# Kernel optimization log

Measured on AMD Instinct MI355X. Metric: run time of the kernel, lower is better.

## Reference

```python
import jax, jax.numpy as jnp
import numpy as np
from jax import lax

B = 8192
HS = 64        # hidden_size (output channels)
HS4 = HS + 4   # internal channel count (68)
K = 3          # conv kernel size


def setup_inputs() -> dict:
    key = jax.random.key(0)
    ks = jax.random.split(key, 16)
    def n(k, shape, s=1.0):
        return jax.random.normal(k, shape, dtype=jnp.float32) * s
    return {
        "x": n(ks[0], (B, HS, 6, 6)),
        "cell": n(ks[1], (B, 2)),
        "interspace_coord": n(ks[2], (B, 2, 6, 6)),
        "conv1_w": n(ks[3], (HS4, HS4, K, K), 0.05),
        "conv1_b": n(ks[4], (HS4,), 0.05),
        "conv3_w": n(ks[5], (HS4, HS4, K, K), 0.05),
        "conv3_b": n(ks[6], (HS4,), 0.05),
        "lin5_w": n(ks[7], (9 * HS, HS4 * 25), 0.02),
        "lin5_b": n(ks[8], (9 * HS,), 0.02),
        "lin4_w": n(ks[9], (9 * HS, HS4 * 16), 0.02),
        "lin4_b": n(ks[10], (9 * HS,), 0.02),
        "lin3_w": n(ks[11], (9 * HS, HS4 * 9), 0.02),
        "lin3_b": n(ks[12], (9 * HS,), 0.02),
        "final_w": n(ks[13], (HS, 9 * HS), 0.02),
        "final_b": n(ks[14], (HS,), 0.02),
    }


def _conv(z, w, b):
    # torch Conv2d with padding=k//2, stride 1 == SAME conv, NCHW/OIHW
    y = lax.conv_general_dilated(z, w, (1, 1), 'SAME',
                                 dimension_numbers=('NCHW', 'OIHW', 'NCHW'))
    return y + b[None, :, None, None]


def _corners(z, ws):
    # four corner windows, stacked on a new leading axis (corner-major)
    H, W = z.shape[-2:]
    return jnp.stack([z[..., :ws, :ws],
                      z[..., :ws, W - ws:],
                      z[..., H - ws:, :ws],
                      z[..., H - ws:, W - ws:]], axis=0)


def reference(x, cell, interspace_coord,
              conv1_w, conv1_b, conv3_w, conv3_b,
              lin5_w, lin5_b, lin4_w, lin4_b, lin3_w, lin3_b,
              final_w, final_b):
    Bn = x.shape[0]
    new_cell = jnp.broadcast_to(cell.reshape(Bn, -1)[:, :, None, None],
                                (Bn, 2, 6, 6))
    lins = {5: (lin5_w, lin5_b), 4: (lin4_w, lin4_b), 3: (lin3_w, lin3_b)}
    for ws in (5, 4, 3):
        z = jnp.concatenate([x, new_cell, interspace_coord], axis=1)  # [B,68,6,6]
        z = _corners(z, ws).reshape(-1, HS4, ws, ws)                  # [4B,68,ws,ws]
        z = jnp.sin(z) + jnp.cos(z)
        z = jax.nn.relu(_conv(z, conv1_w, conv1_b))
        z = jnp.sin(z) + jnp.cos(z)
        z = jax.nn.relu(_conv(z, conv3_w, conv3_b)).reshape(4, Bn, -1)
        Wl, bl = lins[ws]
        z = jax.nn.relu(z @ Wl.T + bl).reshape(4, Bn, HS, 3, 3)
        m = jnp.concatenate([z[0], z[1]], axis=-1)   # [B,64,3,6]
        n = jnp.concatenate([z[2], z[3]], axis=-1)
        x = jnp.concatenate([m, n], axis=-2)          # [B,64,6,6]
    ew = 3
    c = _corners(x, ew)                               # [4,B,64,3,3]
    c = c.reshape(4 * Bn, -1) @ final_w.T + final_b   # [4B,64]
    c = c.reshape(Bn, HS, 2, 2)                       # same flat-order reshape as torch
    xc = x[:, :, ew - 1:ew + 1, ew - 1:ew + 1]        # center 2x2
    return (xc * c).reshape(Bn, HS, -1)
```

## Files before the change

kernel.cpp:

```cpp
#include <hip/hip_runtime.h>
#include <hip/hip_bf16.h>
#include <cstdint>
#include <cstddef>

#define BN 8192
#define MTOT 32768

using bf16 = __hip_bfloat16;
typedef float f32x4 __attribute__((ext_vector_type(4)));
typedef short short8 __attribute__((ext_vector_type(8)));

__device__ __forceinline__ bf16 f2b(float v) { return __float2bfloat16(v); }
__device__ __forceinline__ float b2f(bf16 v) { return __bfloat162float(v); }
__device__ __forceinline__ float sincos_sum(float x) {
    return 1.41421356237f * __sinf(x + 0.78539816340f);
}

template<int WS> struct WsCfg;
template<> struct WsCfg<5> { static constexpr int KD = 1728, NP = 1792, KTRUE = 1700; };
template<> struct WsCfg<4> { static constexpr int KD = 1088, NP = 1152, KTRUE = 1088; };
template<> struct WsCfg<3> { static constexpr int KD = 640,  NP = 640,  KTRUE = 612;  };

template<int WS, bool SRC_F32>
__global__ __launch_bounds__(256)
void zprep_block(const float* __restrict__ xF, const bf16* __restrict__ xB,
                 const float* __restrict__ cell, const float* __restrict__ isc,
                 bf16* __restrict__ Z, int m0g, int CM)
{
    constexpr int KD = WsCfg<WS>::KD;
    constexpr int KTRUE = 68 * WS * WS;
    const int b = blockIdx.x, tid = threadIdx.x;
    __shared__ float s[68][37];

    for (int i = tid; i < 64 * 36; i += 256) {
        int ic = i / 36, off = i % 36;
        size_t idx = ((size_t)b * 64 + ic) * 36 + off;
        float t = SRC_F32 ? xF[idx] : b2f(xB[idx]);
        s[ic][off] = sincos_sum(t);
    }
    if (tid < 2) {
        float t = sincos_sum(cell[b * 2 + tid]);
        #pragma unroll
        for (int off = 0; off < 36; off++) s[64 + tid][off] = t;
    }
    if (tid >= 64 && tid < 136) {
        int j = tid - 64;
        int ic = j / 36, off = j % 36;
        s[66 + ic][off] = sincos_sum(isc[((size_t)b * 2 + ic) * 36 + off]);
    }
    __syncthreads();

    for (int i = tid; i < 4 * KD; i += 256) {
        int q = i / KD, k = i % KD;
        int gm = q * BN + b;
        if (gm < m0g || gm >= m0g + CM) continue;
        float v = 0.f;
        if (k < KTRUE) {
            int pi = k / 68, ic = k % 68;
            int r = (q >> 1) * (6 - WS) + pi / WS;
            int c = (q & 1) * (6 - WS) + pi % WS;
            v = s[ic][r * 6 + c];
        }
        Z[(size_t)(gm - m0g) * KD + k] = f2b(v);
    }
}

template<int WS>
__global__ void build_wdense(const float* __restrict__ w1, const float* __restrict__ w3,
                             bf16* __restrict__ W1d, bf16* __restrict__ W3d)
{
    constexpr int KD = WsCfg<WS>::KD, NP = WsCfg<WS>::NP;
    constexpr int KTRUE = 68 * WS * WS;
    constexpr unsigned per = (unsigned)NP * (unsigned)KD;
    unsigned e = blockIdx.x * 256u + threadIdx.x;
    if (e >= 2u * per) return;
    const float* src = (e < per) ? w1 : w3;
    bf16* dst = (e < per) ? W1d : W3d;
    unsigned i = (e < per) ? e : (e - per);
    int n = (int)(i / (unsigned)KD), k = (int)(i % (unsigned)KD);
    float v = 0.f;
    if (n < KTRUE && k < KTRUE) {
        int po = n / 68, oc = n % 68, ro = po / WS, co = po % WS;
        int pi = k / 68, ic = k % 68, ri = pi / WS, ci = pi % WS;
        int kr = ri - ro + 1, kc = ci - co + 1;
        if (kr >= 0 && kr < 3 && kc >= 0 && kc < 3)
            v = src[((oc * 68 + ic) * 3 + kr) * 3 + kc];
    }
    dst[i] = f2b(v);
}

template<int WS>
__global__ void repack_lin(const float* __restrict__ wl, bf16* __restrict__ WlP)
{
    constexpr int KD = WsCfg<WS>::KD;
    constexpr int KTRUE = 68 * WS * WS;
    unsigned e = blockIdx.x * 256u + threadIdx.x;
    if (e >= 640u * (unsigned)KD) return;
    int n = (int)(e / (unsigned)KD), k = (int)(e % (unsigned)KD);
    float v = 0.f;
    if (n < 576 && k < KTRUE) {
        int pi = k / 68, ic = k % 68;
        v = wl[(size_t)n * KTRUE + ic * (WS * WS) + pi];
    }
    WlP[e] = f2b(v);
}

__global__ void repack_fin(const float* __restrict__ fw, bf16* __restrict__ WfP)
{
    unsigned e = blockIdx.x * 256u + threadIdx.x;
    if (e >= 128u * 576u) return;
    unsigned n = e / 576u, k = e % 576u;
    WfP[e] = (n < 64u) ? f2b(fw[n * 576u + k]) : f2b(0.f);
}

__global__ void build_bias(const float* __restrict__ b1, const float* __restrict__ b3,
                           const float* __restrict__ bl5, const float* __restrict__ bl4,
                           const float* __restrict__ bl3, const float* __restrict__ bfin,
                           float* __restrict__ bias)
{
    int e = blockIdx.x * 256 + threadIdx.x;
    if (e >= 9216) return;
    float v = 0.f;
    if (e < 1792)      { int n = e;        if (n < 1700) v = b1[n % 68]; }
    else if (e < 3584) { int n = e - 1792; if (n < 1700) v = b3[n % 68]; }
    else if (e < 4736) { int n = e - 3584; if (n < 1088) v = b1[n % 68]; }
    else if (e < 5888) { int n = e - 4736; if (n < 1088) v = b3[n % 68]; }
    else if (e < 6528) { int n = e - 5888; if (n < 612)  v = b1[n % 68]; }
    else if (e < 7168) { int n = e - 6528; if (n < 612)  v = b3[n % 68]; }
    else if (e < 7808) { int n = e - 7168; if (n < 576)  v = bl5[n]; }
    else if (e < 8448) { int n = e - 7808; if (n < 576)  v = bl4[n]; }
    else if (e < 9088) { int n = e - 8448; if (n < 576)  v = bl3[n]; }
    else               { int n = e - 9088; if (n < 64)   v = bfin[n]; }
    bias[e] = v;
}

__device__ __forceinline__ void gload_lds16(const bf16* g, const bf16* lds_wave_base)
{
    unsigned off = (unsigned)(uintptr_t)lds_wave_base;
    off = __builtin_amdgcn_readfirstlane(off);
    __builtin_amdgcn_global_load_lds((const __attribute__((address_space(1))) unsigned int*)g,
                                     (__attribute__((address_space(3))) unsigned int*)off,
                                     16, 0, 0);
}

__device__ __forceinline__ int imin(int a, int b) { return a < b ? a : b; }
__device__ __forceinline__ int imax(int a, int b) { return a > b ? a : b; }

template<int EPI, int WS>
__global__ __launch_bounds__(256)
void gemm_bt(const bf16* __restrict__ A, const bf16* __restrict__ Bm, int KD,
             const float* __restrict__ bias, int ntiles,
             bf16* __restrict__ C, int ldc, int nlimit,
             int m0g, bf16* __restrict__ xbuf_out,
             const bf16* __restrict__ afin_xc, float* __restrict__ outp)
{
    __shared__ bf16 As[128 * 32];
    __shared__ bf16 Bs[128 * 32];
    const int tid = threadIdx.x;
    const int wave = tid >> 6, lane = tid & 63;
    const int l15 = lane & 15, lq = lane >> 4;
    const int wr = (wave >> 1) * 64, wc = (wave & 1) * 64;

    const int id = blockIdx.x;
    const int mt8 = (int)gridDim.x / (ntiles * 8);
    const int xcd = id & 7, local = id >> 3;
    const int m_idx = xcd * mt8 + local / ntiles;
    const int n_idx = local % ntiles;
    const int n0 = n_idx * 128, m0 = m_idx * 128;

    int nspans = 1, sbeg[4], send[4];
    sbeg[0] = 0; send[0] = KD;
    if (WS > 0) {
        int po_lo = imin(n0 / 68, WS * WS - 1);
        int po_hi = imin((n0 + 127) / 68, WS * WS - 1);
        int ro_lo = po_lo / WS, ro_hi = po_hi / WS;
        int r_lo = imax(ro_lo - 1, 0), r_hi = imin(ro_hi + 1, WS - 1);
        int ci_lo = 0, ci_hi = WS - 1;
        if (ro_lo == ro_hi) {
            ci_lo = imax(po_lo % WS - 1, 0);
            ci_hi = imin(po_hi % WS + 1, WS - 1);
        }
        if (ci_lo == 0 && ci_hi == WS - 1) {
            sbeg[0] = (r_lo * WS * 68) & ~31;
            send[0] = imin(KD, ((r_hi + 1) * WS * 68 + 31) & ~31);
        } else {
            nspans = 0;
            for (int ri = r_lo; ri <= r_hi; ri++) {
                sbeg[nspans] = ((ri * WS + ci_lo) * 68) & ~31;
                send[nspans] = imin(KD, (((ri * WS + ci_hi + 1) * 68) + 31) & ~31);
                nspans++;
            }
        }
    }

    float bj[4];
    #pragma unroll
    for (int j = 0; j < 4; j++) bj[j] = bias[n0 + wc + j * 16 + l15];

    const bf16* Ab = A + (size_t)m0 * KD;
    const bf16* Bb = Bm + (size_t)n0 * KD;
    const int srow = tid >> 2, scol = (tid & 3) * 8;
    const bf16* aG0 = Ab + (size_t)srow * KD + scol;
    const bf16* aG1 = Ab + (size_t)(srow + 64) * KD + scol;
    const bf16* bG0 = Bb + (size_t)srow * KD + scol;
    const bf16* bG1 = Bb + (size_t)(srow + 64) * KD + scol;
    const bf16* lA0 = &As[wave * 512];
    const bf16* lA1 = &As[2048 + wave * 512];
    const bf16* lB0 = &Bs[wave * 512];
    const bf16* lB1 = &Bs[2048 + wave * 512];

    f32x4 acc[4][4];
    #pragma unroll
    for (int i = 0; i < 4; i++)
        #pragma unroll
        for (int j = 0; j < 4; j++) { f32x4 z = {0.f, 0.f, 0.f, 0.f}; acc[i][j] = z; }

    for (int s = 0; s < nspans; s++) {
        for (int k0 = sbeg[s]; k0 < send[s]; k0 += 32) {
            gload_lds16(aG0 + k0, lA0);
            gload_lds16(aG1 + k0, lA1);
            gload_lds16(bG0 + k0, lB0);
            gload_lds16(bG1 + k0, lB1);
            __syncthreads();
            short8 af[4], bg[4];
            #pragma unroll
            for (int i = 0; i < 4; i++) af[i] = *(const short8*)&As[(wr + i * 16 + l15) * 32 + lq * 8];
            #pragma unroll
            for (int j = 0; j < 4; j++) bg[j] = *(const short8*)&Bs[(wc + j * 16 + l15) * 32 + lq * 8];
            #pragma unroll
            for (int i = 0; i < 4; i++)
                #pragma unroll
                for (int j = 0; j < 4; j++)
                    acc[i][j] = __builtin_amdgcn_mfma_f32_16x16x32_bf16(af[i], bg[j], acc[i][j], 0, 0, 0);
            __syncthreads();
        }
    }

    #pragma unroll
    for (int i = 0; i < 4; i++) {
        #pragma unroll
        for (int j = 0; j < 4; j++) {
            int n = n0 + wc + j * 16 + l15;
            #pragma unroll
            for (int r = 0; r < 4; r++) {
                int m = m0 + wr + i * 16 + lq * 4 + r;
                float v = acc[i][j][r];
                if (EPI == 0) {
                    if (n < nlimit) {
                        v += bj[j]; v = fmaxf(v, 0.f); v = sincos_sum(v);
                        C[(size_t)m * ldc + n] = f2b(v);
                    }
                } else if (EPI == 1) {
                    if (n < nlimit) {
                        v += bj[j]; v = fmaxf(v, 0.f);
                        C[(size_t)m * ldc + n] = f2b(v);
                    }
                } else if (EPI == 2) {
                    if (n < 576) {
                        v += bj[j]; v = fmaxf(v, 0.f);
                        int gm = m0g + m;
                        int q = gm >> 13, b = gm & (BN - 1);
                        int ch = n / 9, p = n % 9, rr = p / 3, cc = p % 3;
                        int R = rr + (q >> 1) * 3, Cc = cc + (q & 1) * 3;
                        xbuf_out[((size_t)b * 64 + ch) * 36 + R * 6 + Cc] = f2b(v);
                    }
                } else {
                    if (n < 64) {
                        v += bj[j];
                        int gm = m0g + m;
                        int f = gm * 64 + n;
                        int b2 = f >> 8, rem = f & 255;
                        int ch2 = rem >> 2, ii = (rem >> 1) & 1, jj = rem & 1;
                        int qq = ii * 2 + jj;
                        const int offt[4] = {8, 6, 2, 0};
                        float xc = b2f(afin_xc[((size_t)qq * BN + b2) * 576 + ch2 * 9 + offt[qq]]);
                        outp[f] = v * xc;
                    }
                }
            }
        }
    }
}

template<int WS, bool SRC_F32>
static void run_ws(const float* xsrcF, const bf16* xsrcB, bf16* xdst, bf16* afin,
                   const float* cell, const float* isc,
                   bf16* Za, bf16* Zb, const bf16* W1d, const bf16* W3d, const bf16* WlP,
                   const float* bias, int bo1, int bo3, int bol,
                   int nchunk, hipStream_t stream)
{
    constexpr int KD = WsCfg<WS>::KD, NP = WsCfg<WS>::NP;
    int CM = MTOT / nchunk;
    int mt = CM / 128;
    for (int c = 0; c < nchunk; c++) {
        int m0g = c * CM;
        zprep_block<WS, SRC_F32><<<BN, 256, 0, stream>>>(
            xsrcF, xsrcB, cell, isc, Za, m0g, CM);
        int nt12 = NP / 128;
        gemm_bt<0, WS><<<nt12 * mt, 256, 0, stream>>>(Za, W1d, KD, bias + bo1, nt12,
                                                      Zb, KD, KD, 0, nullptr, nullptr, nullptr);
        gemm_bt<1, WS><<<nt12 * mt, 256, 0, stream>>>(Zb, W3d, KD, bias + bo3, nt12,
                                                      Za, KD, KD, 0, nullptr, nullptr, nullptr);
        if (afin) {
            gemm_bt<1, 0><<<5 * mt, 256, 0, stream>>>(Za, WlP, KD, bias + bol, 5,
                                                      afin + (size_t)m0g * 576, 576, 576,
                                                      0, nullptr, nullptr, nullptr);
        } else {
            gemm_bt<2, 0><<<5 * mt, 256, 0, stream>>>(Za, WlP, KD, bias + bol, 5,
                                                      nullptr, 0, 0, m0g, xdst, nullptr, nullptr);
        }
    }
}

extern "C" void kernel_launch(void* const* d_in, const int* in_sizes, int n_in,
                              void* d_out, int out_size, void* d_ws, size_t ws_size,
                              hipStream_t stream)
{
    const float* x    = (const float*)d_in[0];
    const float* cell = (const float*)d_in[1];
    const float* isc  = (const float*)d_in[2];
    const float* c1w  = (const float*)d_in[3];
    const float* c1b  = (const float*)d_in[4];
    const float* c3w  = (const float*)d_in[5];
    const float* c3b  = (const float*)d_in[6];
    const float* l5w  = (const float*)d_in[7];
    const float* l5b  = (const float*)d_in[8];
    const float* l4w  = (const float*)d_in[9];
    const float* l4b  = (const float*)d_in[10];
    const float* l3w  = (const float*)d_in[11];
    const float* l3b  = (const float*)d_in[12];
    const float* fw   = (const float*)d_in[13];
    const float* fb   = (const float*)d_in[14];

    char* base = (char*)d_ws;
    size_t cur = 0;
    auto take = [&](size_t bytes) -> char* {
        char* r = base + cur; cur += (bytes + 255) & ~(size_t)255; return r;
    };

    const size_t XB = (size_t)BN * 64 * 36 * 2;
    const size_t AFB = (size_t)MTOT * 576 * 2;
    size_t wbytes = 2 * (1792ull * 1728 + 1152ull * 1088 + 640ull * 640) * 2
                  + (640ull * 1728 + 640ull * 1088 + 640ull * 640) * 2
                  + 128ull * 576 * 2 + 9216ull * 4 + 64 * 256;
    auto need = [&](int nc) -> size_t {
        size_t xb = (nc > 1) ? 2 * XB : XB;
        return xb + AFB + wbytes + 2 * ((size_t)(MTOT / nc) * 1728 * 2);
    };
    int nchunk = (ws_size >= need(1)) ? 1 : (ws_size >= need(2)) ? 2
               : (ws_size >= need(4)) ? 4 : 8;

    bf16* xbufA = (bf16*)take(XB);
    bf16* xbufB = (nchunk > 1) ? (bf16*)take(XB) : xbufA;
    bf16* afinb = (bf16*)take(AFB);
    bf16* w1d5 = (bf16*)take(1792ull * 1728 * 2);
    bf16* w3d5 = (bf16*)take(1792ull * 1728 * 2);
    bf16* w1d4 = (bf16*)take(1152ull * 1088 * 2);
    bf16* w3d4 = (bf16*)take(1152ull * 1088 * 2);
    bf16* w1d3 = (bf16*)take(640ull * 640 * 2);
    bf16* w3d3 = (bf16*)take(640ull * 640 * 2);
    bf16* wl5p = (bf16*)take(640ull * 1728 * 2);
    bf16* wl4p = (bf16*)take(640ull * 1088 * 2);
    bf16* wl3p = (bf16*)take(640ull * 640 * 2);
    bf16* wfp  = (bf16*)take(128ull * 576 * 2);
    float* biasb = (float*)take(9216ull * 4);
    int CM = MTOT / nchunk;
    bf16* Za = (bf16*)take((size_t)CM * 1728 * 2);
    bf16* Zb = (bf16*)take((size_t)CM * 1728 * 2);

    auto nb = [](size_t t) { return dim3((unsigned)((t + 255) / 256)); };
    build_wdense<5><<<nb(2ull * 1792 * 1728), 256, 0, stream>>>(c1w, c3w, w1d5, w3d5);
    build_wdense<4><<<nb(2ull * 1152 * 1088), 256, 0, stream>>>(c1w, c3w, w1d4, w3d4);
    build_wdense<3><<<nb(2ull * 640 * 640), 256, 0, stream>>>(c1w, c3w, w1d3, w3d3);
    repack_lin<5><<<nb(640ull * 1728), 256, 0, stream>>>(l5w, wl5p);
    repack_lin<4><<<nb(640ull * 1088), 256, 0, stream>>>(l4w, wl4p);
    repack_lin<3><<<nb(640ull * 640), 256, 0, stream>>>(l3w, wl3p);
    repack_fin<<<nb(128ull * 576), 256, 0, stream>>>(fw, wfp);
    build_bias<<<36, 256, 0, stream>>>(c1b, c3b, l5b, l4b, l3b, fb, biasb);

    run_ws<5, true >(x, nullptr, xbufA, nullptr, cell, isc, Za, Zb, w1d5, w3d5, wl5p,
                     biasb, 0, 1792, 7168, nchunk, stream);
    run_ws<4, false>(nullptr, xbufA, xbufB, nullptr, cell, isc, Za, Zb, w1d4, w3d4, wl4p,
                     biasb, 3584, 4736, 7808, nchunk, stream);
    run_ws<3, false>(nullptr, xbufB, nullptr, afinb, cell, isc, Za, Zb, w1d3, w3d3, wl3p,
                     biasb, 5888, 6528, 8448, nchunk, stream);

    for (int c = 0; c < nchunk; c++) {
        int m0g = c * CM;
        int mt = CM / 128;
        gemm_bt<3, 0><<<mt, 256, 0, stream>>>(afinb + (size_t)m0g * 576, wfp, 576,
                                              biasb + 9088, 1, nullptr, 0, 0, m0g,
                                              nullptr, afinb, (float*)d_out);
    }
}
```

Before: 1.340 ms.

## Scatter linear epilogue directly into next stage's im2col buffer, merge setup kernels

```diff
diff --git a/kernel.cpp b/kernel.cpp
--- a/kernel.cpp
+++ b/kernel.cpp
@@ -21,22 +21,18 @@
 template<> struct WsCfg<4> { static constexpr int KD = 1088, NP = 1152, KTRUE = 1088; };
 template<> struct WsCfg<3> { static constexpr int KD = 640,  NP = 640,  KTRUE = 612;  };
 
-template<int WS, bool SRC_F32>
 __global__ __launch_bounds__(256)
-void zprep_block(const float* __restrict__ xF, const bf16* __restrict__ xB,
-                 const float* __restrict__ cell, const float* __restrict__ isc,
-                 bf16* __restrict__ Z, int m0g, int CM)
-{
-    constexpr int KD = WsCfg<WS>::KD;
-    constexpr int KTRUE = 68 * WS * WS;
+void zprep_block(const float* __restrict__ xF, const float* __restrict__ cell,
+                 const float* __restrict__ isc, bf16* __restrict__ Z,
+                 int m0g, int CM)
+{
+    constexpr int KD = 1728, KTRUE = 1700;
     const int b = blockIdx.x, tid = threadIdx.x;
     __shared__ float s[68][37];
 
     for (int i = tid; i < 64 * 36; i += 256) {
         int ic = i / 36, off = i % 36;
-        size_t idx = ((size_t)b * 64 + ic) * 36 + off;
-        float t = SRC_F32 ? xF[idx] : b2f(xB[idx]);
-        s[ic][off] = sincos_sum(t);
+        s[ic][off] = sincos_sum(xF[((size_t)b * 64 + ic) * 36 + off]);
     }
     if (tid < 2) {
         float t = sincos_sum(cell[b * 2 + tid]);
@@ -57,81 +53,136 @@
         float v = 0.f;
         if (k < KTRUE) {
             int pi = k / 68, ic = k % 68;
-            int r = (q >> 1) * (6 - WS) + pi / WS;
-            int c = (q & 1) * (6 - WS) + pi % WS;
+            int r = (q >> 1) + pi / 5;
+            int c = (q & 1) + pi % 5;
             v = s[ic][r * 6 + c];
         }
         Z[(size_t)(gm - m0g) * KD + k] = f2b(v);
     }
 }
 
-template<int WS>
-__global__ void build_wdense(const float* __restrict__ w1, const float* __restrict__ w3,
-                             bf16* __restrict__ W1d, bf16* __restrict__ W3d)
-{
-    constexpr int KD = WsCfg<WS>::KD, NP = WsCfg<WS>::NP;
-    constexpr int KTRUE = 68 * WS * WS;
-    constexpr unsigned per = (unsigned)NP * (unsigned)KD;
-    unsigned e = blockIdx.x * 256u + threadIdx.x;
-    if (e >= 2u * per) return;
-    const float* src = (e < per) ? w1 : w3;
-    bf16* dst = (e < per) ? W1d : W3d;
-    unsigned i = (e < per) ? e : (e - per);
-    int n = (int)(i / (unsigned)KD), k = (int)(i % (unsigned)KD);
+template<int WSv>
+__device__ __forceinline__ bf16 conv_elem(const float* __restrict__ src, int n, int k)
+{
+    constexpr int KTRUE = 68 * WSv * WSv;
     float v = 0.f;
     if (n < KTRUE && k < KTRUE) {
-        int po = n / 68, oc = n % 68, ro = po / WS, co = po % WS;
-        int pi = k / 68, ic = k % 68, ri = pi / WS, ci = pi % WS;
+        int po = n / 68, oc = n % 68, ro = po / WSv, co = po % WSv;
+        int pi = k / 68, ic = k % 68, ri = pi / WSv, ci = pi % WSv;
         int kr = ri - ro + 1, kc = ci - co + 1;
         if (kr >= 0 && kr < 3 && kc >= 0 && kc < 3)
             v = src[((oc * 68 + ic) * 3 + kr) * 3 + kc];
     }
-    dst[i] = f2b(v);
-}
-
-template<int WS>
-__global__ void repack_lin(const float* __restrict__ wl, bf16* __restrict__ WlP)
-{
-    constexpr int KD = WsCfg<WS>::KD;
-    constexpr int KTRUE = 68 * WS * WS;
-    unsigned e = blockIdx.x * 256u + threadIdx.x;
-    if (e >= 640u * (unsigned)KD) return;
-    int n = (int)(e / (unsigned)KD), k = (int)(e % (unsigned)KD);
+    return f2b(v);
+}
+template<int WSv>
+__device__ __forceinline__ bf16 lin_elem(const float* __restrict__ wl, int n, int k)
+{
+    constexpr int KTRUE = 68 * WSv * WSv;
     float v = 0.f;
     if (n < 576 && k < KTRUE) {
         int pi = k / 68, ic = k % 68;
-        v = wl[(size_t)n * KTRUE + ic * (WS * WS) + pi];
-    }
-    WlP[e] = f2b(v);
-}
-
-__global__ void repack_fin(const float* __restrict__ fw, bf16* __restrict__ WfP)
-{
+        v = wl[(size_t)n * KTRUE + ic * (WSv * WSv) + pi];
+    }
+    return f2b(v);
+}
+
+__global__ void megabuild(const float* __restrict__ c1w, const float* __restrict__ c3w,
+                          const float* __restrict__ l5w, const float* __restrict__ l4w,
+                          const float* __restrict__ l3w, const float* __restrict__ fw,
+                          const float* __restrict__ c1b, const float* __restrict__ c3b,
+                          const float* __restrict__ bl5, const float* __restrict__ bl4,
+                          const float* __restrict__ bl3, const float* __restrict__ bfin,
+                          const float* __restrict__ cell, const float* __restrict__ isc,
+                          bf16* __restrict__ w1d5, bf16* __restrict__ w3d5,
+                          bf16* __restrict__ w1d4, bf16* __restrict__ w3d4,
+                          bf16* __restrict__ w1d3, bf16* __restrict__ w3d3,
+                          bf16* __restrict__ wl5p, bf16* __restrict__ wl4p,
+                          bf16* __restrict__ wl3p, bf16* __restrict__ wfp,
+                          float* __restrict__ bias,
+                          bf16* __restrict__ Z4, bf16* __restrict__ Z3)
+{
+    constexpr unsigned S0 = 2u*1792*1728, S1 = 2u*1152*1088, S2 = 2u*640*640;
+    constexpr unsigned S3 = 640u*1728, S4 = 640u*1088, S5 = 640u*640;
+    constexpr unsigned S6 = 128u*576, S7 = 9216;
+    constexpr unsigned S8 = 4u*8192*16*4, S9 = 4u*8192*9*4, S10 = 32768u*28;
+    constexpr unsigned O1=S0, O2=O1+S1, O3=O2+S2, O4=O3+S3, O5=O4+S4, O6=O5+S5,
+                       O7=O6+S6, O8=O7+S7, O9=O8+S8, O10=O9+S9, OT=O10+S10;
     unsigned e = blockIdx.x * 256u + threadIdx.x;
-    if (e >= 128u * 576u) return;
-    unsigned n = e / 576u, k = e % 576u;
-    WfP[e] = (n < 64u) ? f2b(fw[n * 576u + k]) : f2b(0.f);
-}
-
-__global__ void build_bias(const float* __restrict__ b1, const float* __restrict__ b3,
-                           const float* __restrict__ bl5, const float* __restrict__ bl4,
-                           const float* __restrict__ bl3, const float* __restrict__ bfin,
-                           float* __restrict__ bias)
-{
-    int e = blockIdx.x * 256 + threadIdx.x;
-    if (e >= 9216) return;
-    float v = 0.f;
-    if (e < 1792)      { int n = e;        if (n < 1700) v = b1[n % 68]; }
-    else if (e < 3584) { int n = e - 1792; if (n < 1700) v = b3[n % 68]; }
-    else if (e < 4736) { int n = e - 3584; if (n < 1088) v = b1[n % 68]; }
-    else if (e < 5888) { int n = e - 4736; if (n < 1088) v = b3[n % 68]; }
-    else if (e < 6528) { int n = e - 5888; if (n < 612)  v = b1[n % 68]; }
-    else if (e < 7168) { int n = e - 6528; if (n < 612)  v = b3[n % 68]; }
-    else if (e < 7808) { int n = e - 7168; if (n < 576)  v = bl5[n]; }
-    else if (e < 8448) { int n = e - 7808; if (n < 576)  v = bl4[n]; }
-    else if (e < 9088) { int n = e - 8448; if (n < 576)  v = bl3[n]; }
-    else               { int n = e - 9088; if (n < 64)   v = bfin[n]; }
-    bias[e] = v;
+    if (e >= OT) return;
+    if (e < O1) {
+        constexpr unsigned per = 1792u*1728;
+        unsigned i = (e < per) ? e : e - per;
+        bf16* dst = (e < per) ? w1d5 : w3d5;
+        const float* src = (e < per) ? c1w : c3w;
+        dst[i] = conv_elem<5>(src, (int)(i / 1728u), (int)(i % 1728u));
+    } else if (e < O2) {
+        unsigned i0 = e - O1; constexpr unsigned per = 1152u*1088;
+        unsigned i = (i0 < per) ? i0 : i0 - per;
+        bf16* dst = (i0 < per) ? w1d4 : w3d4;
+        const float* src = (i0 < per) ? c1w : c3w;
+        dst[i] = conv_elem<4>(src, (int)(i / 1088u), (int)(i % 1088u));
+    } else if (e < O3) {
+        unsigned i0 = e - O2; constexpr unsigned per = 640u*640;
+        unsigned i = (i0 < per) ? i0 : i0 - per;
+        bf16* dst = (i0 < per) ? w1d3 : w3d3;
+        const float* src = (i0 < per) ? c1w : c3w;
+        dst[i] = conv_elem<3>(src, (int)(i / 640u), (int)(i % 640u));
+    } else if (e < O4) {
+        unsigned i = e - O3;
+        wl5p[i] = lin_elem<5>(l5w, (int)(i / 1728u), (int)(i % 1728u));
+    } else if (e < O5) {
+        unsigned i = e - O4;
+        wl4p[i] = lin_elem<4>(l4w, (int)(i / 1088u), (int)(i % 1088u));
+    } else if (e < O6) {
+        unsigned i = e - O5;
+        wl3p[i] = lin_elem<3>(l3w, (int)(i / 640u), (int)(i % 640u));
+    } else if (e < O7) {
+        unsigned i = e - O6, n = i / 576u, k = i % 576u;
+        wfp[i] = (n < 64u) ? f2b(fw[n * 576u + k]) : f2b(0.f);
+    } else if (e < O8) {
+        int i = (int)(e - O7);
+        float v = 0.f;
+        if (i < 1792)      { int n = i;        if (n < 1700) v = c1b[n % 68]; }
+        else if (i < 3584) { int n = i - 1792; if (n < 1700) v = c3b[n % 68]; }
+        else if (i < 4736) { int n = i - 3584; if (n < 1088) v = c1b[n % 68]; }
+        else if (i < 5888) { int n = i - 4736; if (n < 1088) v = c3b[n % 68]; }
+        else if (i < 6528) { int n = i - 5888; if (n < 612)  v = c1b[n % 68]; }
+        else if (i < 7168) { int n = i - 6528; if (n < 612)  v = c3b[n % 68]; }
+        else if (i < 7808) { int n = i - 7168; if (n < 576)  v = bl5[n]; }
+        else if (i < 8448) { int n = i - 7808; if (n < 576)  v = bl4[n]; }
+        else if (i < 9088) { int n = i - 8448; if (n < 576)  v = bl3[n]; }
+        else               { int n = i - 9088; if (n < 64)   v = bfin[n]; }
+        bias[i] = v;
+    } else if (e < O9) {
+        unsigned i = e - O8;
+        int j = (int)(i & 3u); i >>= 2;
+        int pi = (int)(i & 15u); i >>= 4;
+        int b = (int)(i & 8191u); int q = (int)(i >> 13);
+        float t;
+        if (j < 2) t = cell[b * 2 + j];
+        else {
+            int r = (q >> 1) * 2 + pi / 4, c = (q & 1) * 2 + pi % 4;
+            t = isc[((size_t)b * 2 + (j - 2)) * 36 + r * 6 + c];
+        }
+        Z4[((size_t)q * BN + b) * 1088 + pi * 68 + 64 + j] = f2b(sincos_sum(t));
+    } else if (e < O10) {
+        unsigned i = e - O9;
+        int j = (int)(i & 3u); i >>= 2;
+        int pi = (int)(i % 9u); i /= 9u;
+        int b = (int)(i & 8191u); int q = (int)(i >> 13);
+        float t;
+        if (j < 2) t = cell[b * 2 + j];
+        else {
+            int r = (q >> 1) * 3 + pi / 3, c = (q & 1) * 3 + pi % 3;
+            t = isc[((size_t)b * 2 + (j - 2)) * 36 + r * 6 + c];
+        }
+        Z3[((size_t)q * BN + b) * 640 + pi * 68 + 64 + j] = f2b(sincos_sum(t));
+    } else {
+        unsigned i = e - O10;
+        int m = (int)(i / 28u), t = (int)(i % 28u);
+        Z3[(size_t)m * 640 + 612 + t] = f2b(0.f);
+    }
 }
 
 __device__ __forceinline__ void gload_lds16(const bf16* g, const bf16* lds_wave_base)
@@ -146,12 +197,12 @@
 __device__ __forceinline__ int imin(int a, int b) { return a < b ? a : b; }
 __device__ __forceinline__ int imax(int a, int b) { return a > b ? a : b; }
 
-template<int EPI, int WS>
+template<int EPI, int WS, int WN>
 __global__ __launch_bounds__(256)
 void gemm_bt(const bf16* __restrict__ A, const bf16* __restrict__ Bm, int KD,
              const float* __restrict__ bias, int ntiles,
              bf16* __restrict__ C, int ldc, int nlimit,
-             int m0g, bf16* __restrict__ xbuf_out,
+             int m0g, bf16* __restrict__ znext,
              const bf16* __restrict__ afin_xc, float* __restrict__ outp)
 {
     __shared__ bf16 As[128 * 32];
@@ -258,11 +309,25 @@
                 } else if (EPI == 2) {
                     if (n < 576) {
                         v += bj[j]; v = fmaxf(v, 0.f);
+                        bf16 t = f2b(sincos_sum(v));
                         int gm = m0g + m;
                         int q = gm >> 13, b = gm & (BN - 1);
-                        int ch = n / 9, p = n % 9, rr = p / 3, cc = p % 3;
-                        int R = rr + (q >> 1) * 3, Cc = cc + (q & 1) * 3;
-                        xbuf_out[((size_t)b * 64 + ch) * 36 + R * 6 + Cc] = f2b(v);
+                        int ch = n / 9, p = n % 9;
+                        int R = p / 3 + (q >> 1) * 3, Cc = p % 3 + (q & 1) * 3;
+                        constexpr int OFF = 6 - WN;
+                        constexpr int KDN = (WN == 4) ? 1088 : 640;
+                        #pragma unroll
+                        for (int qr = 0; qr < 2; qr++) {
+                            int rr = R - OFF * qr;
+                            if (rr < 0 || rr >= WN) continue;
+                            #pragma unroll
+                            for (int qc = 0; qc < 2; qc++) {
+                                int cc = Cc - OFF * qc;
+                                if (cc < 0 || cc >= WN) continue;
+                                int pi = rr * WN + cc;
+                                znext[((size_t)((qr * 2 + qc) * BN + b)) * KDN + pi * 68 + ch] = t;
+                            }
+                        }
                     }
                 } else {
                     if (n < 64) {
@@ -282,36 +347,6 @@
     }
 }
 
-template<int WS, bool SRC_F32>
-static void run_ws(const float* xsrcF, const bf16* xsrcB, bf16* xdst, bf16* afin,
-                   const float* cell, const float* isc,
-                   bf16* Za, bf16* Zb, const bf16* W1d, const bf16* W3d, const bf16* WlP,
-                   const float* bias, int bo1, int bo3, int bol,
-                   int nchunk, hipStream_t stream)
-{
-    constexpr int KD = WsCfg<WS>::KD, NP = WsCfg<WS>::NP;
-    int CM = MTOT / nchunk;
-    int mt = CM / 128;
-    for (int c = 0; c < nchunk; c++) {
-        int m0g = c * CM;
-        zprep_block<WS, SRC_F32><<<BN, 256, 0, stream>>>(
-            xsrcF, xsrcB, cell, isc, Za, m0g, CM);
-        int nt12 = NP / 128;
-        gemm_bt<0, WS><<<nt12 * mt, 256, 0, stream>>>(Za, W1d, KD, bias + bo1, nt12,
-                                                      Zb, KD, KD, 0, nullptr, nullptr, nullptr);
-        gemm_bt<1, WS><<<nt12 * mt, 256, 0, stream>>>(Zb, W3d, KD, bias + bo3, nt12,
-                                                      Za, KD, KD, 0, nullptr, nullptr, nullptr);
-        if (afin) {
-            gemm_bt<1, 0><<<5 * mt, 256, 0, stream>>>(Za, WlP, KD, bias + bol, 5,
-                                                      afin + (size_t)m0g * 576, 576, 576,
-                                                      0, nullptr, nullptr, nullptr);
-        } else {
-            gemm_bt<2, 0><<<5 * mt, 256, 0, stream>>>(Za, WlP, KD, bias + bol, 5,
-                                                      nullptr, 0, 0, m0g, xdst, nullptr, nullptr);
-        }
-    }
-}
-
 extern "C" void kernel_launch(void* const* d_in, const int* in_sizes, int n_in,
                               void* d_out, int out_size, void* d_ws, size_t ws_size,
                               hipStream_t stream)
@@ -338,20 +373,20 @@
         char* r = base + cur; cur += (bytes + 255) & ~(size_t)255; return r;
     };
 
-    const size_t XB = (size_t)BN * 64 * 36 * 2;
+    const size_t Z4B = (size_t)MTOT * 1088 * 2;
+    const size_t Z3B = (size_t)MTOT * 640 * 2;
     const size_t AFB = (size_t)MTOT * 576 * 2;
     size_t wbytes = 2 * (1792ull * 1728 + 1152ull * 1088 + 640ull * 640) * 2
                   + (640ull * 1728 + 640ull * 1088 + 640ull * 640) * 2
                   + 128ull * 576 * 2 + 9216ull * 4 + 64 * 256;
     auto need = [&](int nc) -> size_t {
-        size_t xb = (nc > 1) ? 2 * XB : XB;
-        return xb + AFB + wbytes + 2 * ((size_t)(MTOT / nc) * 1728 * 2);
+        return Z4B + Z3B + AFB + wbytes + 2 * ((size_t)(MTOT / nc) * 1728 * 2);
     };
     int nchunk = (ws_size >= need(1)) ? 1 : (ws_size >= need(2)) ? 2
-               : (ws_size >= need(4)) ? 4 : 8;
-
-    bf16* xbufA = (bf16*)take(XB);
-    bf16* xbufB = (nchunk > 1) ? (bf16*)take(XB) : xbufA;
+               : (ws_size >= need(4)) ? 4 : (ws_size >= need(8)) ? 8 : 16;
+
+    bf16* Z4   = (bf16*)take(Z4B);
+    bf16* Z3   = (bf16*)take(Z3B);
     bf16* afinb = (bf16*)take(AFB);
     bf16* w1d5 = (bf16*)take(1792ull * 1728 * 2);
     bf16* w3d5 = (bf16*)take(1792ull * 1728 * 2);
@@ -365,31 +400,54 @@
     bf16* wfp  = (bf16*)take(128ull * 576 * 2);
     float* biasb = (float*)take(9216ull * 4);
     int CM = MTOT / nchunk;
+    int mt = CM / 128;
     bf16* Za = (bf16*)take((size_t)CM * 1728 * 2);
     bf16* Zb = (bf16*)take((size_t)CM * 1728 * 2);
 
-    auto nb = [](size_t t) { return dim3((unsigned)((t + 255) / 256)); };
-    build_wdense<5><<<nb(2ull * 1792 * 1728), 256, 0, stream>>>(c1w, c3w, w1d5, w3d5);
-    build_wdense<4><<<nb(2ull * 1152 * 1088), 256, 0, stream>>>(c1w, c3w, w1d4, w3d4);
-    build_wdense<3><<<nb(2ull * 640 * 640), 256, 0, stream>>>(c1w, c3w, w1d3, w3d3);
-    repack_lin<5><<<nb(640ull * 1728), 256, 0, stream>>>(l5w, wl5p);
-    repack_lin<4><<<nb(640ull * 1088), 256, 0, stream>>>(l4w, wl4p);
-    repack_lin<3><<<nb(640ull * 640), 256, 0, stream>>>(l3w, wl3p);
-    repack_fin<<<nb(128ull * 576), 256, 0, stream>>>(fw, wfp);
-    build_bias<<<36, 256, 0, stream>>>(c1b, c3b, l5b, l4b, l3b, fb, biasb);
-
-    run_ws<5, true >(x, nullptr, xbufA, nullptr, cell, isc, Za, Zb, w1d5, w3d5, wl5p,
-                     biasb, 0, 1792, 7168, nchunk, stream);
-    run_ws<4, false>(nullptr, xbufA, xbufB, nullptr, cell, isc, Za, Zb, w1d4, w3d4, wl4p,
-                     biasb, 3584, 4736, 7808, nchunk, stream);
-    run_ws<3, false>(nullptr, xbufB, nullptr, afinb, cell, isc, Za, Zb, w1d3, w3d3, wl3p,
-                     biasb, 5888, 6528, 8448, nchunk, stream);
+    {
+        constexpr unsigned OT = 2u*1792*1728 + 2u*1152*1088 + 2u*640*640
+                              + 640u*1728 + 640u*1088 + 640u*640 + 128u*576 + 9216
+                              + 4u*8192*16*4 + 4u*8192*9*4 + 32768u*28;
+        megabuild<<<(OT + 255) / 256, 256, 0, stream>>>(
+            c1w, c3w, l5w, l4w, l3w, fw, c1b, c3b, l5b, l4b, l3b, fb, cell, isc,
+            w1d5, w3d5, w1d4, w3d4, w1d3, w3d3, wl5p, wl4p, wl3p, wfp, biasb, Z4, Z3);
+    }
 
     for (int c = 0; c < nchunk; c++) {
         int m0g = c * CM;
-        int mt = CM / 128;
-        gemm_bt<3, 0><<<mt, 256, 0, stream>>>(afinb + (size_t)m0g * 576, wfp, 576,
-                                              biasb + 9088, 1, nullptr, 0, 0, m0g,
-                                              nullptr, afinb, (float*)d_out);
-    }
-}
+        zprep_block<<<BN, 256, 0, stream>>>(x, cell, isc, Za, m0g, CM);
+        gemm_bt<0, 5, 0><<<14 * mt, 256, 0, stream>>>(Za, w1d5, 1728, biasb + 0, 14,
+                                                      Zb, 1728, 1728, 0, nullptr, nullptr, nullptr);
+        gemm_bt<1, 5, 0><<<14 * mt, 256, 0, stream>>>(Zb, w3d5, 1728, biasb + 1792, 14,
+                                                      Za, 1728, 1728, 0, nullptr, nullptr, nullptr);
+        gemm_bt<2, 0, 4><<<5 * mt, 256, 0, stream>>>(Za, wl5p, 1728, biasb + 7168, 5,
+                                                     nullptr, 0, 0, m0g, Z4, nullptr, nullptr);
+    }
+    for (int c = 0; c < nchunk; c++) {
+        int m0g = c * CM;
+        gemm_bt<0, 4, 0><<<9 * mt, 256, 0, stream>>>(Z4 + (size_t)m0g * 1088, w1d4, 1088,
+                                                     biasb + 3584, 9, Zb, 1088, 1088,
+                                                     0, nullptr, nullptr, nullptr);
+        gemm_bt<1, 4, 0><<<9 * mt, 256, 0, stream>>>(Zb, w3d4, 1088, biasb + 4736, 9,
+                                                     Za, 1088, 1088, 0, nullptr, nullptr, nullptr);
+        gemm_bt<2, 0, 3><<<5 * mt, 256, 0, stream>>>(Za, wl4p, 1088, biasb + 7808, 5,
+                                                     nullptr, 0, 0, m0g, Z3, nullptr, nullptr);
+    }
+    for (int c = 0; c < nchunk; c++) {
+        int m0g = c * CM;
+        gemm_bt<0, 3, 0><<<5 * mt, 256, 0, stream>>>(Z3 + (size_t)m0g * 640, w1d3, 640,
+                                                     biasb + 5888, 5, Zb, 640, 640,
+                                                     0, nullptr, nullptr, nullptr);
+        gemm_bt<1, 3, 0><<<5 * mt, 256, 0, stream>>>(Zb, w3d3, 640, biasb + 6528, 5,
+                                                     Za, 640, 640, 0, nullptr, nullptr, nullptr);
+        gemm_bt<1, 0, 0><<<5 * mt, 256, 0, stream>>>(Za, wl3p, 640, biasb + 8448, 5,
+                                                     afinb + (size_t)m0g * 576, 576, 576,
+                                                     0, nullptr, nullptr, nullptr);
+    }
+    for (int c = 0; c < nchunk; c++) {
+        int m0g = c * CM;
+        gemm_bt<3, 0, 0><<<mt, 256, 0, stream>>>(afinb + (size_t)m0g * 576, wfp, 576,
+                                                 biasb + 9088, 1, nullptr, 0, 0, m0g,
+                                                 nullptr, afinb, (float*)d_out);
+    }
+}
```

New measurement: 1.340 ms. About the same (-0.0%).
